# Kernel optimization log

Measured on AMD Instinct MI355X. Metric: run time of the kernel, lower is better.

## Reference

```python
import jax, jax.numpy as jnp
import numpy as np

B = 128          # batch of predictions
C = 1024         # number of constraints
N = 512          # number of atoms appearing in constraints (minimal subset)
NUM_CLASSES = 1024
BODY_P = 0.02    # body sparsity


def setup_inputs() -> dict:
    rng = np.random.default_rng(0)
    # distinct sorted atom indices into the full class space
    atoms = np.sort(rng.permutation(NUM_CLASSES)[:N]).astype(np.int64)
    # each constraint has one head literal: one-hot in pos_head OR neg_head
    head_atom = rng.integers(0, N, size=C)
    head_sign = rng.random(C) < 0.5
    pos_head = np.zeros((C, N), np.float32)
    neg_head = np.zeros((C, N), np.float32)
    rows = np.arange(C)
    pos_head[rows[head_sign], head_atom[head_sign]] = 1.0
    neg_head[rows[~head_sign], head_atom[~head_sign]] = 1.0
    # sparse disjoint 0/1 body masks, head atom excluded from its own body
    pos_body = (rng.random((C, N)) < BODY_P).astype(np.float32)
    neg_body = ((rng.random((C, N)) < BODY_P) & (pos_body == 0)).astype(np.float32)
    pos_body[rows, head_atom] = 0.0
    neg_body[rows, head_atom] = 0.0
    key = jax.random.key(0)
    preds = jax.random.uniform(key, (B, NUM_CLASSES), dtype=jnp.float32)  # probs in [0,1]
    return {
        "preds": preds,
        "pos_head": jnp.asarray(pos_head),
        "neg_head": jnp.asarray(neg_head),
        "pos_body": jnp.asarray(pos_body),
        "neg_body": jnp.asarray(neg_body),
        "atoms": jnp.asarray(atoms),
    }


def reference(preds, pos_head, neg_head, pos_body, neg_body, atoms):
    # to_minimal: gather atom subset  [B, N]
    m = preds[:, atoms]
    # body_rev[b,c,j] = pos_body + m*(neg_body - pos_body)
    #   = (1-m) where body literal positive, m where negative, 0 otherwise
    body_rev = pos_body[None] + m[:, None, :] * (neg_body - pos_body)[None]  # [B,C,N]
    # candidate body satisfaction degree per constraint
    body_min = 1.0 - jnp.max(body_rev, axis=2)  # [B,C]
    # scatter candidates to head atoms via one-hot head masks (max-reduce over cons)
    lb = jnp.max(body_min[:, :, None] * pos_head[None], axis=1)        # [B,N]
    ub = 1.0 - jnp.max(body_min[:, :, None] * neg_head[None], axis=1)  # [B,N]
    lo = jnp.minimum(lb, ub)
    hi = jnp.maximum(lb, ub)
    updated = jnp.maximum(lo, jnp.minimum(hi, m))
    # from_minimal: scatter updated atoms back into full prediction vector
    return preds.at[:, atoms].set(updated)
```

## Files before the change

### kernel.cpp

```cpp
#include <hip/hip_runtime.h>

#define Bsz 128
#define Csz 1024
#define Nsz 512
#define NCsz 1024
#define CAP 64

__global__ __launch_bounds__(256) void k_pre(
    const float* __restrict__ preds,
    const float* __restrict__ pos_head, const float* __restrict__ neg_head,
    const float* __restrict__ pos_body, const float* __restrict__ neg_body,
    const int* __restrict__ atoms,
    float* __restrict__ mT, unsigned* __restrict__ lbmax, unsigned* __restrict__ ubmax,
    int* __restrict__ pos_list, int* __restrict__ neg_list,
    int* __restrict__ pos_cnt, int* __restrict__ neg_cnt,
    int* __restrict__ head_n, int* __restrict__ head_sign)
{
    int blk = blockIdx.x;
    if (blk < 128) {
        int q = blk * 256 + threadIdx.x;
        ((uint4*)lbmax)[q] = make_uint4(0u, 0u, 0u, 0u);
    } else if (blk < 384) {
        int g = (blk - 128) * 256 + threadIdx.x;
        int b = g >> 9, n = g & 511;
        mT[n * Bsz + b] = preds[b * NCsz + atoms[n]];
    } else {
        __shared__ int cnts[4][2];
        int wave = threadIdx.x >> 6, lane = threadIdx.x & 63;
        int c = (blk - 384) * 4 + wave;
        if (lane == 0) { cnts[wave][0] = 0; cnts[wave][1] = 0; }
        const float4* pb4 = (const float4*)(pos_body + c * Nsz);
        const float4* nb4 = (const float4*)(neg_body + c * Nsz);
        const float4* ph4 = (const float4*)(pos_head + c * Nsz);
        const float4* nh4 = (const float4*)(neg_head + c * Nsz);
        for (int k = 0; k < 2; k++) {
            int q = k * 64 + lane;
            float4 p  = pb4[q];
            float4 nb = nb4[q];
            float4 ph = ph4[q];
            float4 nh = nh4[q];
            int n0 = q * 4;
            if (p.x != 0.f) { int s = atomicAdd(&cnts[wave][0], 1); if (s < CAP) pos_list[c * CAP + s] = n0; }
            if (p.y != 0.f) { int s = atomicAdd(&cnts[wave][0], 1); if (s < CAP) pos_list[c * CAP + s] = n0 + 1; }
            if (p.z != 0.f) { int s = atomicAdd(&cnts[wave][0], 1); if (s < CAP) pos_list[c * CAP + s] = n0 + 2; }
            if (p.w != 0.f) { int s = atomicAdd(&cnts[wave][0], 1); if (s < CAP) pos_list[c * CAP + s] = n0 + 3; }
            if (nb.x != 0.f) { int s = atomicAdd(&cnts[wave][1], 1); if (s < CAP) neg_list[c * CAP + s] = n0; }
            if (nb.y != 0.f) { int s = atomicAdd(&cnts[wave][1], 1); if (s < CAP) neg_list[c * CAP + s] = n0 + 1; }
            if (nb.z != 0.f) { int s = atomicAdd(&cnts[wave][1], 1); if (s < CAP) neg_list[c * CAP + s] = n0 + 2; }
            if (nb.w != 0.f) { int s = atomicAdd(&cnts[wave][1], 1); if (s < CAP) neg_list[c * CAP + s] = n0 + 3; }
            if (ph.x != 0.f) { head_n[c] = n0;     head_sign[c] = 1; }
            if (ph.y != 0.f) { head_n[c] = n0 + 1; head_sign[c] = 1; }
            if (ph.z != 0.f) { head_n[c] = n0 + 2; head_sign[c] = 1; }
            if (ph.w != 0.f) { head_n[c] = n0 + 3; head_sign[c] = 1; }
            if (nh.x != 0.f) { head_n[c] = n0;     head_sign[c] = 0; }
            if (nh.y != 0.f) { head_n[c] = n0 + 1; head_sign[c] = 0; }
            if (nh.z != 0.f) { head_n[c] = n0 + 2; head_sign[c] = 0; }
            if (nh.w != 0.f) { head_n[c] = n0 + 3; head_sign[c] = 0; }
        }
        if (lane == 0) {
            pos_cnt[c] = min(cnts[wave][0], CAP);
            neg_cnt[c] = min(cnts[wave][1], CAP);
        }
    }
}

__global__ __launch_bounds__(128) void k_body(
    const float* __restrict__ mT,
    const int* __restrict__ pos_list, const int* __restrict__ neg_list,
    const int* __restrict__ pos_cnt, const int* __restrict__ neg_cnt,
    const int* __restrict__ head_n, const int* __restrict__ head_sign,
    unsigned* __restrict__ lbmax, unsigned* __restrict__ ubmax)
{
    int c = blockIdx.x, b = threadIdx.x;
    int pc = pos_cnt[c], ncnt = neg_cnt[c];
    const int* pl = pos_list + c * CAP;
    const int* nl = neg_list + c * CAP;
    float acc = 0.f;
    for (int e = 0; e < pc; e++)   acc = fmaxf(acc, 1.f - mT[pl[e] * Bsz + b]);
    for (int e = 0; e < ncnt; e++) acc = fmaxf(acc, mT[nl[e] * Bsz + b]);
    float bm = 1.f - acc;
    unsigned* dst = head_sign[c] ? lbmax : ubmax;
    atomicMax(dst + head_n[c] * Bsz + b, __float_as_uint(bm));
}

__global__ __launch_bounds__(256) void k_final(
    const float* __restrict__ preds,
    const float* __restrict__ mT,
    const unsigned* __restrict__ lbmax, const unsigned* __restrict__ ubmax,
    const int* __restrict__ atoms, float* __restrict__ out)
{
    int blk = blockIdx.x, tid = threadIdx.x;
    if (blk < 256) {
        int t = blk * 256 + tid;
        int b = t & 127, n = t >> 7;
        int i = n * Bsz + b;
        float m  = mT[i];
        float lb = __uint_as_float(lbmax[i]);
        float ub = 1.f - __uint_as_float(ubmax[i]);
        float lo = fminf(lb, ub), hi = fmaxf(lb, ub);
        out[b * NCsz + atoms[n]] = fmaxf(lo, fminf(hi, m));
    } else {
        __shared__ int la[Nsz];
        for (int i = tid; i < Nsz; i += 256) la[i] = atoms[i];
        __syncthreads();
        int t = (blk - 256) * 256 + tid;
        int b = t >> 10, j = t & 1023;
        int lo = 0, hi = Nsz;
        while (lo < hi) { int mid = (lo + hi) >> 1; if (la[mid] < j) lo = mid + 1; else hi = mid; }
        bool isatom = (lo < Nsz) && (la[lo] == j);
        if (!isatom) out[b * NCsz + j] = preds[b * NCsz + j];
    }
}

extern "C" void kernel_launch(void* const* d_in, const int* in_sizes, int n_in,
                              void* d_out, int out_size, void* d_ws, size_t ws_size,
                              hipStream_t stream)
{
    const float* preds    = (const float*)d_in[0];
    const float* pos_head = (const float*)d_in[1];
    const float* neg_head = (const float*)d_in[2];
    const float* pos_body = (const float*)d_in[3];
    const float* neg_body = (const float*)d_in[4];
    const int*   atoms    = (const int*)d_in[5];
    float* out = (float*)d_out;

    char* ws = (char*)d_ws;
    float*    mT        = (float*)(ws);
    unsigned* lbmax     = (unsigned*)(ws + 65536u  * 4);
    unsigned* ubmax     = (unsigned*)(ws + 131072u * 4);
    int*      pos_list  = (int*)(ws + 196608u * 4);
    int*      neg_list  = (int*)(ws + 262144u * 4);
    int*      pos_cnt   = (int*)(ws + 327680u * 4);
    int*      neg_cnt   = pos_cnt + Csz;
    int*      head_n    = neg_cnt + Csz;
    int*      head_sign = head_n + Csz;

    k_pre<<<640, 256, 0, stream>>>(preds, pos_head, neg_head, pos_body, neg_body, atoms,
                                   mT, lbmax, ubmax, pos_list, neg_list,
                                   pos_cnt, neg_cnt, head_n, head_sign);

    k_body<<<Csz, Bsz, 0, stream>>>(mT, pos_list, neg_list, pos_cnt, neg_cnt,
                                    head_n, head_sign, lbmax, ubmax);

    k_final<<<768, 256, 0, stream>>>(preds, mT, lbmax, ubmax, atoms, out);
}
```

Before: 77.63 us.

## Fuse three kernels into one cooperative kernel with grid syncs

The three kernels (preprocessing, body evaluation, final write) become one cooperative kernel of 256 blocks by 512 threads, separated by grid-wide syncs. Each block keeps its four constraints' literal lists in shared memory, so the global pos/neg list and count buffers disappear. The final stage uses a shared inverse-atom table instead of a binary search and writes each output element once. This removes two kernel launches and their gaps, plus global round trips for the lists, at the cost of two grid barriers and a cooperative launch.

```diff
diff --git a/kernel.cpp b/kernel.cpp
--- a/kernel.cpp
+++ b/kernel.cpp
@@ -1,114 +1,107 @@
 #include <hip/hip_runtime.h>
+#include <hip/hip_cooperative_groups.h>
+
+namespace cg = cooperative_groups;
 
 #define Bsz 128
 #define Csz 1024
 #define Nsz 512
 #define NCsz 1024
 #define CAP 64
+#define NBLK 256
+#define NTHR 512
 
-__global__ __launch_bounds__(256) void k_pre(
+__global__ __launch_bounds__(NTHR) void k_fused(
     const float* __restrict__ preds,
     const float* __restrict__ pos_head, const float* __restrict__ neg_head,
     const float* __restrict__ pos_body, const float* __restrict__ neg_body,
     const int* __restrict__ atoms,
-    float* __restrict__ mT, unsigned* __restrict__ lbmax, unsigned* __restrict__ ubmax,
-    int* __restrict__ pos_list, int* __restrict__ neg_list,
-    int* __restrict__ pos_cnt, int* __restrict__ neg_cnt,
-    int* __restrict__ head_n, int* __restrict__ head_sign)
+    float* __restrict__ mT,
+    unsigned* __restrict__ bounds,
+    float* __restrict__ out)
 {
-    int blk = blockIdx.x;
-    if (blk < 128) {
-        int q = blk * 256 + threadIdx.x;
-        ((uint4*)lbmax)[q] = make_uint4(0u, 0u, 0u, 0u);
-    } else if (blk < 384) {
-        int g = (blk - 128) * 256 + threadIdx.x;
-        int b = g >> 9, n = g & 511;
-        mT[n * Bsz + b] = preds[b * NCsz + atoms[n]];
-    } else {
-        __shared__ int cnts[4][2];
-        int wave = threadIdx.x >> 6, lane = threadIdx.x & 63;
-        int c = (blk - 384) * 4 + wave;
-        if (lane == 0) { cnts[wave][0] = 0; cnts[wave][1] = 0; }
-        const float4* pb4 = (const float4*)(pos_body + c * Nsz);
-        const float4* nb4 = (const float4*)(neg_body + c * Nsz);
-        const float4* ph4 = (const float4*)(pos_head + c * Nsz);
-        const float4* nh4 = (const float4*)(neg_head + c * Nsz);
-        for (int k = 0; k < 2; k++) {
-            int q = k * 64 + lane;
-            float4 p  = pb4[q];
-            float4 nb = nb4[q];
-            float4 ph = ph4[q];
-            float4 nh = nh4[q];
-            int n0 = q * 4;
-            if (p.x != 0.f) { int s = atomicAdd(&cnts[wave][0], 1); if (s < CAP) pos_list[c * CAP + s] = n0; }
-            if (p.y != 0.f) { int s = atomicAdd(&cnts[wave][0], 1); if (s < CAP) pos_list[c * CAP + s] = n0 + 1; }
-            if (p.z != 0.f) { int s = atomicAdd(&cnts[wave][0], 1); if (s < CAP) pos_list[c * CAP + s] = n0 + 2; }
-            if (p.w != 0.f) { int s = atomicAdd(&cnts[wave][0], 1); if (s < CAP) pos_list[c * CAP + s] = n0 + 3; }
-            if (nb.x != 0.f) { int s = atomicAdd(&cnts[wave][1], 1); if (s < CAP) neg_list[c * CAP + s] = n0; }
-            if (nb.y != 0.f) { int s = atomicAdd(&cnts[wave][1], 1); if (s < CAP) neg_list[c * CAP + s] = n0 + 1; }
-            if (nb.z != 0.f) { int s = atomicAdd(&cnts[wave][1], 1); if (s < CAP) neg_list[c * CAP + s] = n0 + 2; }
-            if (nb.w != 0.f) { int s = atomicAdd(&cnts[wave][1], 1); if (s < CAP) neg_list[c * CAP + s] = n0 + 3; }
-            if (ph.x != 0.f) { head_n[c] = n0;     head_sign[c] = 1; }
-            if (ph.y != 0.f) { head_n[c] = n0 + 1; head_sign[c] = 1; }
-            if (ph.z != 0.f) { head_n[c] = n0 + 2; head_sign[c] = 1; }
-            if (ph.w != 0.f) { head_n[c] = n0 + 3; head_sign[c] = 1; }
-            if (nh.x != 0.f) { head_n[c] = n0;     head_sign[c] = 0; }
-            if (nh.y != 0.f) { head_n[c] = n0 + 1; head_sign[c] = 0; }
-            if (nh.z != 0.f) { head_n[c] = n0 + 2; head_sign[c] = 0; }
-            if (nh.w != 0.f) { head_n[c] = n0 + 3; head_sign[c] = 0; }
+    __shared__ int   plist[4][CAP];
+    __shared__ int   nlist[4][CAP];
+    __shared__ int   cnts[4][2];
+    __shared__ int   headn[4];
+    __shared__ int   headsg[4];
+    __shared__ short inv[NCsz];
+
+    cg::grid_group grid = cg::this_grid();
+    const int g   = blockIdx.x;
+    const int tid = threadIdx.x;
+
+    unsigned* lbmax = bounds;
+    unsigned* ubmax = bounds + Bsz * Nsz;
+
+    if (tid < 8) cnts[tid >> 1][tid & 1] = 0;
+    inv[2 * tid]     = -1;
+    inv[2 * tid + 1] = -1;
+    __syncthreads();
+
+    inv[atoms[tid]] = (short)tid;
+
+    bounds[g * NTHR + tid] = 0u;
+
+    if (tid < 2 * Bsz) {
+        int col = 2 * g + (tid >> 7);
+        int b   = tid & (Bsz - 1);
+        mT[col * Bsz + b] = preds[b * NCsz + atoms[col]];
+    }
+
+    {
+        int cl = tid >> 7, q = tid & 127;
+        int c  = 4 * g + cl;
+        int n0 = q * 4;
+        float4 p  = ((const float4*)(pos_body + c * Nsz))[q];
+        float4 nb = ((const float4*)(neg_body + c * Nsz))[q];
+        float4 ph = ((const float4*)(pos_head + c * Nsz))[q];
+        float4 nh = ((const float4*)(neg_head + c * Nsz))[q];
+        if (p.x  != 0.f) { int s = atomicAdd(&cnts[cl][0], 1); if (s < CAP) plist[cl][s] = n0;     }
+        if (p.y  != 0.f) { int s = atomicAdd(&cnts[cl][0], 1); if (s < CAP) plist[cl][s] = n0 + 1; }
+        if (p.z  != 0.f) { int s = atomicAdd(&cnts[cl][0], 1); if (s < CAP) plist[cl][s] = n0 + 2; }
+        if (p.w  != 0.f) { int s = atomicAdd(&cnts[cl][0], 1); if (s < CAP) plist[cl][s] = n0 + 3; }
+        if (nb.x != 0.f) { int s = atomicAdd(&cnts[cl][1], 1); if (s < CAP) nlist[cl][s] = n0;     }
+        if (nb.y != 0.f) { int s = atomicAdd(&cnts[cl][1], 1); if (s < CAP) nlist[cl][s] = n0 + 1; }
+        if (nb.z != 0.f) { int s = atomicAdd(&cnts[cl][1], 1); if (s < CAP) nlist[cl][s] = n0 + 2; }
+        if (nb.w != 0.f) { int s = atomicAdd(&cnts[cl][1], 1); if (s < CAP) nlist[cl][s] = n0 + 3; }
+        if (ph.x != 0.f) { headn[cl] = n0;     headsg[cl] = 1; }
+        if (ph.y != 0.f) { headn[cl] = n0 + 1; headsg[cl] = 1; }
+        if (ph.z != 0.f) { headn[cl] = n0 + 2; headsg[cl] = 1; }
+        if (ph.w != 0.f) { headn[cl] = n0 + 3; headsg[cl] = 1; }
+        if (nh.x != 0.f) { headn[cl] = n0;     headsg[cl] = 0; }
+        if (nh.y != 0.f) { headn[cl] = n0 + 1; headsg[cl] = 0; }
+        if (nh.z != 0.f) { headn[cl] = n0 + 2; headsg[cl] = 0; }
+        if (nh.w != 0.f) { headn[cl] = n0 + 3; headsg[cl] = 0; }
+    }
+
+    grid.sync();
+
+    {
+        int cl = tid >> 7, b = tid & 127;
+        int pc = min(cnts[cl][0], CAP);
+        int nc = min(cnts[cl][1], CAP);
+        float acc = 0.f;
+        for (int e = 0; e < pc; e++) acc = fmaxf(acc, 1.f - mT[plist[cl][e] * Bsz + b]);
+        for (int e = 0; e < nc; e++) acc = fmaxf(acc, mT[nlist[cl][e] * Bsz + b]);
+        unsigned* dst = headsg[cl] ? lbmax : ubmax;
+        atomicMax(dst + headn[cl] * Bsz + b, __float_as_uint(1.f - acc));
+    }
+
+    grid.sync();
+
+    {
+        int t = g * NTHR + tid;
+        int b = t >> 10, j = t & (NCsz - 1);
+        float v = preds[b * NCsz + j];
+        int n = inv[j];
+        if (n >= 0) {
+            float lb = __uint_as_float(lbmax[n * Bsz + b]);
+            float ub = 1.f - __uint_as_float(ubmax[n * Bsz + b]);
+            float lo = fminf(lb, ub), hi = fmaxf(lb, ub);
+            v = fmaxf(lo, fminf(hi, v));
         }
-        if (lane == 0) {
-            pos_cnt[c] = min(cnts[wave][0], CAP);
-            neg_cnt[c] = min(cnts[wave][1], CAP);
-        }
-    }
-}
-
-__global__ __launch_bounds__(128) void k_body(
-    const float* __restrict__ mT,
-    const int* __restrict__ pos_list, const int* __restrict__ neg_list,
-    const int* __restrict__ pos_cnt, const int* __restrict__ neg_cnt,
-    const int* __restrict__ head_n, const int* __restrict__ head_sign,
-    unsigned* __restrict__ lbmax, unsigned* __restrict__ ubmax)
-{
-    int c = blockIdx.x, b = threadIdx.x;
-    int pc = pos_cnt[c], ncnt = neg_cnt[c];
-    const int* pl = pos_list + c * CAP;
-    const int* nl = neg_list + c * CAP;
-    float acc = 0.f;
-    for (int e = 0; e < pc; e++)   acc = fmaxf(acc, 1.f - mT[pl[e] * Bsz + b]);
-    for (int e = 0; e < ncnt; e++) acc = fmaxf(acc, mT[nl[e] * Bsz + b]);
-    float bm = 1.f - acc;
-    unsigned* dst = head_sign[c] ? lbmax : ubmax;
-    atomicMax(dst + head_n[c] * Bsz + b, __float_as_uint(bm));
-}
-
-__global__ __launch_bounds__(256) void k_final(
-    const float* __restrict__ preds,
-    const float* __restrict__ mT,
-    const unsigned* __restrict__ lbmax, const unsigned* __restrict__ ubmax,
-    const int* __restrict__ atoms, float* __restrict__ out)
-{
-    int blk = blockIdx.x, tid = threadIdx.x;
-    if (blk < 256) {
-        int t = blk * 256 + tid;
-        int b = t & 127, n = t >> 7;
-        int i = n * Bsz + b;
-        float m  = mT[i];
-        float lb = __uint_as_float(lbmax[i]);
-        float ub = 1.f - __uint_as_float(ubmax[i]);
-        float lo = fminf(lb, ub), hi = fmaxf(lb, ub);
-        out[b * NCsz + atoms[n]] = fmaxf(lo, fminf(hi, m));
-    } else {
-        __shared__ int la[Nsz];
-        for (int i = tid; i < Nsz; i += 256) la[i] = atoms[i];
-        __syncthreads();
-        int t = (blk - 256) * 256 + tid;
-        int b = t >> 10, j = t & 1023;
-        int lo = 0, hi = Nsz;
-        while (lo < hi) { int mid = (lo + hi) >> 1; if (la[mid] < j) lo = mid + 1; else hi = mid; }
-        bool isatom = (lo < Nsz) && (la[lo] == j);
-        if (!isatom) out[b * NCsz + j] = preds[b * NCsz + j];
+        out[b * NCsz + j] = v;
     }
 }
 
@@ -125,22 +118,14 @@
     float* out = (float*)d_out;
 
     char* ws = (char*)d_ws;
-    float*    mT        = (float*)(ws);
-    unsigned* lbmax     = (unsigned*)(ws + 65536u  * 4);
-    unsigned* ubmax     = (unsigned*)(ws + 131072u * 4);
-    int*      pos_list  = (int*)(ws + 196608u * 4);
-    int*      neg_list  = (int*)(ws + 262144u * 4);
-    int*      pos_cnt   = (int*)(ws + 327680u * 4);
-    int*      neg_cnt   = pos_cnt + Csz;
-    int*      head_n    = neg_cnt + Csz;
-    int*      head_sign = head_n + Csz;
+    float*    mT     = (float*)ws;
+    unsigned* bounds = (unsigned*)(ws + 65536u * 4);
 
-    k_pre<<<640, 256, 0, stream>>>(preds, pos_head, neg_head, pos_body, neg_body, atoms,
-                                   mT, lbmax, ubmax, pos_list, neg_list,
-                                   pos_cnt, neg_cnt, head_n, head_sign);
-
-    k_body<<<Csz, Bsz, 0, stream>>>(mT, pos_list, neg_list, pos_cnt, neg_cnt,
-                                    head_n, head_sign, lbmax, ubmax);
-
-    k_final<<<768, 256, 0, stream>>>(preds, mT, lbmax, ubmax, atoms, out);
+    void* args[] = {
+        (void*)&preds, (void*)&pos_head, (void*)&neg_head,
+        (void*)&pos_body, (void*)&neg_body, (void*)&atoms,
+        (void*)&mT, (void*)&bounds, (void*)&out
+    };
+    hipLaunchCooperativeKernel((const void*)k_fused, dim3(NBLK), dim3(NTHR),
+                               args, 0, stream);
 }
```

After: 140.3 us. +80.7%, slower.

## Fuse body evaluation into per-atom apply kernel, dropping atomics and lb/ub buffers

Applied to the files above, without the earlier changes.

Merges the per-constraint body kernel and the final kernel into one per-atom kernel. Each block scans the head table to find the constraints whose head is its atom, evaluates those bodies, and reduces lb/ub in shared memory. This removes one launch, the zeroing of the lb/ub buffers and the global atomicMax scatter. The binary search for non-atom columns is replaced by a shared-memory isatom bitmap. The cost is that every block scans all 1024 head entries, and constraints per atom are capped at 32, which could silently drop matches on other inputs.

```diff
diff --git a/kernel.cpp b/kernel.cpp
--- a/kernel.cpp
+++ b/kernel.cpp
@@ -5,29 +5,28 @@
 #define Nsz 512
 #define NCsz 1024
 #define CAP 64
+#define MCAP 32
+#define NT2 512
 
-__global__ __launch_bounds__(256) void k_pre(
+__global__ __launch_bounds__(256) void k_scan(
     const float* __restrict__ preds,
     const float* __restrict__ pos_head, const float* __restrict__ neg_head,
     const float* __restrict__ pos_body, const float* __restrict__ neg_body,
     const int* __restrict__ atoms,
-    float* __restrict__ mT, unsigned* __restrict__ lbmax, unsigned* __restrict__ ubmax,
+    float* __restrict__ mT,
     int* __restrict__ pos_list, int* __restrict__ neg_list,
     int* __restrict__ pos_cnt, int* __restrict__ neg_cnt,
-    int* __restrict__ head_n, int* __restrict__ head_sign)
+    int* __restrict__ head_of)
 {
-    int blk = blockIdx.x;
-    if (blk < 128) {
-        int q = blk * 256 + threadIdx.x;
-        ((uint4*)lbmax)[q] = make_uint4(0u, 0u, 0u, 0u);
-    } else if (blk < 384) {
-        int g = (blk - 128) * 256 + threadIdx.x;
-        int b = g >> 9, n = g & 511;
-        mT[n * Bsz + b] = preds[b * NCsz + atoms[n]];
+    int blk = blockIdx.x, tid = threadIdx.x;
+    if (blk < 256) {
+        int b   = tid & (Bsz - 1);
+        int col = 2 * blk + (tid >> 7);
+        mT[col * Bsz + b] = preds[b * NCsz + atoms[col]];
     } else {
         __shared__ int cnts[4][2];
-        int wave = threadIdx.x >> 6, lane = threadIdx.x & 63;
-        int c = (blk - 384) * 4 + wave;
+        int wave = tid >> 6, lane = tid & 63;
+        int c = (blk - 256) * 4 + wave;
         if (lane == 0) { cnts[wave][0] = 0; cnts[wave][1] = 0; }
         const float4* pb4 = (const float4*)(pos_body + c * Nsz);
         const float4* nb4 = (const float4*)(neg_body + c * Nsz);
@@ -40,22 +39,22 @@
             float4 ph = ph4[q];
             float4 nh = nh4[q];
             int n0 = q * 4;
-            if (p.x != 0.f) { int s = atomicAdd(&cnts[wave][0], 1); if (s < CAP) pos_list[c * CAP + s] = n0; }
-            if (p.y != 0.f) { int s = atomicAdd(&cnts[wave][0], 1); if (s < CAP) pos_list[c * CAP + s] = n0 + 1; }
-            if (p.z != 0.f) { int s = atomicAdd(&cnts[wave][0], 1); if (s < CAP) pos_list[c * CAP + s] = n0 + 2; }
-            if (p.w != 0.f) { int s = atomicAdd(&cnts[wave][0], 1); if (s < CAP) pos_list[c * CAP + s] = n0 + 3; }
-            if (nb.x != 0.f) { int s = atomicAdd(&cnts[wave][1], 1); if (s < CAP) neg_list[c * CAP + s] = n0; }
+            if (p.x  != 0.f) { int s = atomicAdd(&cnts[wave][0], 1); if (s < CAP) pos_list[c * CAP + s] = n0;     }
+            if (p.y  != 0.f) { int s = atomicAdd(&cnts[wave][0], 1); if (s < CAP) pos_list[c * CAP + s] = n0 + 1; }
+            if (p.z  != 0.f) { int s = atomicAdd(&cnts[wave][0], 1); if (s < CAP) pos_list[c * CAP + s] = n0 + 2; }
+            if (p.w  != 0.f) { int s = atomicAdd(&cnts[wave][0], 1); if (s < CAP) pos_list[c * CAP + s] = n0 + 3; }
+            if (nb.x != 0.f) { int s = atomicAdd(&cnts[wave][1], 1); if (s < CAP) neg_list[c * CAP + s] = n0;     }
             if (nb.y != 0.f) { int s = atomicAdd(&cnts[wave][1], 1); if (s < CAP) neg_list[c * CAP + s] = n0 + 1; }
             if (nb.z != 0.f) { int s = atomicAdd(&cnts[wave][1], 1); if (s < CAP) neg_list[c * CAP + s] = n0 + 2; }
             if (nb.w != 0.f) { int s = atomicAdd(&cnts[wave][1], 1); if (s < CAP) neg_list[c * CAP + s] = n0 + 3; }
-            if (ph.x != 0.f) { head_n[c] = n0;     head_sign[c] = 1; }
-            if (ph.y != 0.f) { head_n[c] = n0 + 1; head_sign[c] = 1; }
-            if (ph.z != 0.f) { head_n[c] = n0 + 2; head_sign[c] = 1; }
-            if (ph.w != 0.f) { head_n[c] = n0 + 3; head_sign[c] = 1; }
-            if (nh.x != 0.f) { head_n[c] = n0;     head_sign[c] = 0; }
-            if (nh.y != 0.f) { head_n[c] = n0 + 1; head_sign[c] = 0; }
-            if (nh.z != 0.f) { head_n[c] = n0 + 2; head_sign[c] = 0; }
-            if (nh.w != 0.f) { head_n[c] = n0 + 3; head_sign[c] = 0; }
+            if (ph.x != 0.f) head_of[c] = ((n0    ) << 1) | 1;
+            if (ph.y != 0.f) head_of[c] = ((n0 + 1) << 1) | 1;
+            if (ph.z != 0.f) head_of[c] = ((n0 + 2) << 1) | 1;
+            if (ph.w != 0.f) head_of[c] = ((n0 + 3) << 1) | 1;
+            if (nh.x != 0.f) head_of[c] = ((n0    ) << 1);
+            if (nh.y != 0.f) head_of[c] = ((n0 + 1) << 1);
+            if (nh.z != 0.f) head_of[c] = ((n0 + 2) << 1);
+            if (nh.w != 0.f) head_of[c] = ((n0 + 3) << 1);
         }
         if (lane == 0) {
             pos_cnt[c] = min(cnts[wave][0], CAP);
@@ -64,51 +63,69 @@
     }
 }
 
-__global__ __launch_bounds__(128) void k_body(
+__global__ __launch_bounds__(NT2) void k_apply(
+    const float* __restrict__ preds,
     const float* __restrict__ mT,
     const int* __restrict__ pos_list, const int* __restrict__ neg_list,
     const int* __restrict__ pos_cnt, const int* __restrict__ neg_cnt,
-    const int* __restrict__ head_n, const int* __restrict__ head_sign,
-    unsigned* __restrict__ lbmax, unsigned* __restrict__ ubmax)
-{
-    int c = blockIdx.x, b = threadIdx.x;
-    int pc = pos_cnt[c], ncnt = neg_cnt[c];
-    const int* pl = pos_list + c * CAP;
-    const int* nl = neg_list + c * CAP;
-    float acc = 0.f;
-    for (int e = 0; e < pc; e++)   acc = fmaxf(acc, 1.f - mT[pl[e] * Bsz + b]);
-    for (int e = 0; e < ncnt; e++) acc = fmaxf(acc, mT[nl[e] * Bsz + b]);
-    float bm = 1.f - acc;
-    unsigned* dst = head_sign[c] ? lbmax : ubmax;
-    atomicMax(dst + head_n[c] * Bsz + b, __float_as_uint(bm));
-}
-
-__global__ __launch_bounds__(256) void k_final(
-    const float* __restrict__ preds,
-    const float* __restrict__ mT,
-    const unsigned* __restrict__ lbmax, const unsigned* __restrict__ ubmax,
-    const int* __restrict__ atoms, float* __restrict__ out)
+    const int* __restrict__ head_of,
+    const int* __restrict__ atoms,
+    float* __restrict__ out)
 {
     int blk = blockIdx.x, tid = threadIdx.x;
-    if (blk < 256) {
-        int t = blk * 256 + tid;
-        int b = t & 127, n = t >> 7;
-        int i = n * Bsz + b;
-        float m  = mT[i];
-        float lb = __uint_as_float(lbmax[i]);
-        float ub = 1.f - __uint_as_float(ubmax[i]);
-        float lo = fminf(lb, ub), hi = fmaxf(lb, ub);
-        out[b * NCsz + atoms[n]] = fmaxf(lo, fminf(hi, m));
+    if (blk < Nsz) {
+        __shared__ int   matched[MCAP];
+        __shared__ int   mcnt;
+        __shared__ float lbs[4][Bsz];
+        __shared__ float ubs[4][Bsz];
+        const int n = blk;
+        if (tid == 0) mcnt = 0;
+        __syncthreads();
+        for (int i = tid; i < Csz; i += NT2) {
+            int h = head_of[i];
+            if ((h >> 1) == n) {
+                int s = atomicAdd(&mcnt, 1);
+                if (s < MCAP) matched[s] = (i << 1) | (h & 1);
+            }
+        }
+        __syncthreads();
+        int q = tid >> 7, b = tid & (Bsz - 1);
+        float lb = 0.f, ubm = 0.f;
+        int mc = min(mcnt, MCAP);
+        for (int k = q; k < mc; k += 4) {
+            int c    = matched[k] >> 1;
+            int sign = matched[k] & 1;
+            const int* pl = pos_list + c * CAP;
+            const int* nl = neg_list + c * CAP;
+            int pc = pos_cnt[c], nc = neg_cnt[c];
+            float acc = 0.f;
+            for (int e = 0; e < pc; e++) acc = fmaxf(acc, 1.f - mT[pl[e] * Bsz + b]);
+            for (int e = 0; e < nc; e++) acc = fmaxf(acc, mT[nl[e] * Bsz + b]);
+            float bm = 1.f - acc;
+            if (sign) lb = fmaxf(lb, bm); else ubm = fmaxf(ubm, bm);
+        }
+        lbs[q][b] = lb; ubs[q][b] = ubm;
+        __syncthreads();
+        if (q == 0) {
+            lb  = fmaxf(fmaxf(lbs[0][b], lbs[1][b]), fmaxf(lbs[2][b], lbs[3][b]));
+            ubm = fmaxf(fmaxf(ubs[0][b], ubs[1][b]), fmaxf(ubs[2][b], ubs[3][b]));
+            float ub = 1.f - ubm;
+            float m  = mT[n * Bsz + b];
+            float lo = fminf(lb, ub), hi = fmaxf(lb, ub);
+            out[b * NCsz + atoms[n]] = fmaxf(lo, fminf(hi, m));
+        }
     } else {
-        __shared__ int la[Nsz];
-        for (int i = tid; i < Nsz; i += 256) la[i] = atoms[i];
+        __shared__ char isatom[NCsz];
+        int p = blk - Nsz;
+        for (int i = tid; i < NCsz; i += NT2) isatom[i] = 0;
         __syncthreads();
-        int t = (blk - 256) * 256 + tid;
-        int b = t >> 10, j = t & 1023;
-        int lo = 0, hi = Nsz;
-        while (lo < hi) { int mid = (lo + hi) >> 1; if (la[mid] < j) lo = mid + 1; else hi = mid; }
-        bool isatom = (lo < Nsz) && (la[lo] == j);
-        if (!isatom) out[b * NCsz + j] = preds[b * NCsz + j];
+        isatom[atoms[tid]] = 1;
+        __syncthreads();
+        for (int k = 0; k < 4; k++) {
+            int t = p * (4 * NT2) + k * NT2 + tid;
+            int b = t >> 10, j = t & (NCsz - 1);
+            if (!isatom[j]) out[b * NCsz + j] = preds[b * NCsz + j];
+        }
     }
 }
 
@@ -125,22 +142,16 @@
     float* out = (float*)d_out;
 
     char* ws = (char*)d_ws;
-    float*    mT        = (float*)(ws);
-    unsigned* lbmax     = (unsigned*)(ws + 65536u  * 4);
-    unsigned* ubmax     = (unsigned*)(ws + 131072u * 4);
-    int*      pos_list  = (int*)(ws + 196608u * 4);
-    int*      neg_list  = (int*)(ws + 262144u * 4);
-    int*      pos_cnt   = (int*)(ws + 327680u * 4);
-    int*      neg_cnt   = pos_cnt + Csz;
-    int*      head_n    = neg_cnt + Csz;
-    int*      head_sign = head_n + Csz;
+    float* mT       = (float*)(ws);
+    int*   pos_list = (int*)(ws + 65536u * 4);
+    int*   neg_list = (int*)(ws + 131072u * 4);
+    int*   pos_cnt  = (int*)(ws + 196608u * 4);
+    int*   neg_cnt  = pos_cnt + Csz;
+    int*   head_of  = neg_cnt + Csz;
 
-    k_pre<<<640, 256, 0, stream>>>(preds, pos_head, neg_head, pos_body, neg_body, atoms,
-                                   mT, lbmax, ubmax, pos_list, neg_list,
-                                   pos_cnt, neg_cnt, head_n, head_sign);
+    k_scan<<<512, 256, 0, stream>>>(preds, pos_head, neg_head, pos_body, neg_body, atoms,
+                                    mT, pos_list, neg_list, pos_cnt, neg_cnt, head_of);
 
-    k_body<<<Csz, Bsz, 0, stream>>>(mT, pos_list, neg_list, pos_cnt, neg_cnt,
-                                    head_n, head_sign, lbmax, ubmax);
-
-    k_final<<<768, 256, 0, stream>>>(preds, mT, lbmax, ubmax, atoms, out);
+    k_apply<<<576, NT2, 0, stream>>>(preds, mT, pos_list, neg_list, pos_cnt, neg_cnt,
+                                     head_of, atoms, out);
 }
```

New measurement: 84.21 us. 1.08x slower.
